# Performance work log

Measured on AMD Instinct MI355X. Metric: run time of the kernel, lower is better.

## Reference

```python
import jax, jax.numpy as jnp
import numpy as np

TOP_K = 8
ROUTED_SCALING = 2.5


def setup_inputs() -> dict:
    key = jax.random.key(0)
    ks = jax.random.split(key, 8)
    B, S, H, E, I = 2, 1024, 2048, 32, 1024
    IS = 2 * I  # shared expert intermediate (n_shared_experts * moe_intermediate_size)
    w = lambda k, shape: jax.random.normal(k, shape, dtype=jnp.float32) * 0.02
    return {
        "hidden_states": jax.random.normal(ks[0], (B, S, H), dtype=jnp.float32),
        "gate_weight": w(ks[1], (E, H)),
        "w_gate": w(ks[2], (E, H, I)),
        "w_up": w(ks[3], (E, H, I)),
        "w_down": w(ks[4], (E, I, H)),
        "ws_gate": w(ks[5], (H, IS)),
        "ws_up": w(ks[6], (H, IS)),
        "ws_down": w(ks[7], (IS, H)),
    }


def reference(hidden_states, gate_weight, w_gate, w_up, w_down, ws_gate, ws_up, ws_down):
    B, S, H = hidden_states.shape
    x = hidden_states.reshape(-1, H)  # [T, H]
    T = x.shape[0]
    E = gate_weight.shape[0]

    # --- gate (DeepseekV3 top-k router: sigmoid scores, top-k, renormalize, scale) ---
    scores = jax.nn.sigmoid(x @ gate_weight.T)              # [T, E]
    topk_w, topk_i = jax.lax.top_k(scores, TOP_K)           # [T, K]
    topk_w = topk_w / (jnp.sum(topk_w, axis=-1, keepdims=True) + 1e-20)
    topk_w = topk_w * ROUTED_SCALING

    # dense [T, E] combine weights (scatter of top-k weights; zeros elsewhere)
    dense_w = jnp.zeros((T, E), dtype=topk_w.dtype).at[
        jnp.arange(T)[:, None], topk_i
    ].add(topk_w)

    # --- all experts on all tokens (calibrate_all_experts semantics; non-selected get weight 0) ---
    g = jnp.einsum('th,ehi->eti', x, w_gate)                # [E, T, I]
    u = jnp.einsum('th,ehi->eti', x, w_up)                  # [E, T, I]
    eo = jnp.einsum('eti,eih->eth', jax.nn.silu(g) * u, w_down)  # [E, T, H]
    routed = jnp.einsum('eth,te->th', eo, dense_w)          # weighted scatter-combine

    # --- shared expert (gated SiLU MLP on residual) ---
    shared = (jax.nn.silu(x @ ws_gate) * (x @ ws_up)) @ ws_down

    return (routed + shared).reshape(B, S, H)
```

## Files before the change

### kernel.cpp

```cpp
#include <hip/hip_runtime.h>

#define T_TOK 2048
#define H_DIM 2048
#define E_NUM 32
#define I_DIM 1024
#define IS_DIM 2048
#define K_TOT (E_NUM * I_DIM + IS_DIM)
#define SLOT_CAP 2048
#define NE_ALL 34
#define GU_TILES 192
#define DN_TILES 176
#define ACT_SLOTS 24576

typedef __bf16 bf16x8 __attribute__((ext_vector_type(8)));
typedef float  f32x4  __attribute__((ext_vector_type(4)));
static_assert(sizeof(bf16x8) == 16, "bf16x8 must be 16B");

#define OFF_CNT   ((size_t)0)
#define OFF_NTGU  ((size_t)192)
#define OFF_NTDN  ((size_t)196)
#define OFF_BASE  ((size_t)256)
#define OFF_TGU   ((size_t)512)
#define OFF_TDN   ((size_t)1280)
#define OFF_PAIRS ((size_t)2048)
#define OFF_XB    ((size_t)280576)
#define OFF_WGT   ((size_t)8669184)
#define OFF_WUT   ((size_t)142886912)
#define OFF_WSGT  ((size_t)277104640)
#define OFF_WSUT  ((size_t)285493248)
#define OFF_WDT   ((size_t)293881856)
#define OFF_ACT   ((size_t)436488192)

__device__ __forceinline__ unsigned short f2bf(float f) {
  unsigned int u = __float_as_uint(f);
  u += 0x7fffu + ((u >> 16) & 1u);
  return (unsigned short)(u >> 16);
}

__device__ __forceinline__ void gld16(const void* g, void* l) {
  __builtin_amdgcn_global_load_lds(
      (const __attribute__((address_space(1))) unsigned int*)g,
      (__attribute__((address_space(3))) unsigned int*)l, 16, 0, 0);
}

__global__ __launch_bounds__(256) void router_kernel(
    const float* __restrict__ x, const float* __restrict__ gw,
    int* __restrict__ cnt, unsigned int* __restrict__ pairs,
    unsigned short* __restrict__ xb)
{
  const int t = blockIdx.x;
  __shared__ float xs[H_DIM];
  __shared__ float sc[E_NUM];
  const float4* xr = (const float4*)(x + (long)t * H_DIM);
  for (int i = threadIdx.x; i < H_DIM / 4; i += 256) ((float4*)xs)[i] = xr[i];
  __syncthreads();
  {
    const int i0 = threadIdx.x * 8;
    ushort4 o1, o2;
    o1.x = f2bf(xs[i0 + 0]); o1.y = f2bf(xs[i0 + 1]);
    o1.z = f2bf(xs[i0 + 2]); o1.w = f2bf(xs[i0 + 3]);
    o2.x = f2bf(xs[i0 + 4]); o2.y = f2bf(xs[i0 + 5]);
    o2.z = f2bf(xs[i0 + 6]); o2.w = f2bf(xs[i0 + 7]);
    *(ushort4*)(xb + (long)t * H_DIM + i0) = o1;
    *(ushort4*)(xb + (long)t * H_DIM + i0 + 4) = o2;
  }
  const int e = threadIdx.x >> 3, p = threadIdx.x & 7;
  const float4* ga = (const float4*)(gw + (long)e * H_DIM);
  const float4* xa = (const float4*)xs;
  float s = 0.f;
  #pragma unroll 4
  for (int i = p * 64; i < p * 64 + 64; ++i) {
    float4 a = ga[i], b = xa[i];
    s += a.x * b.x + a.y * b.y + a.z * b.z + a.w * b.w;
  }
  s += __shfl_down(s, 4, 8);
  s += __shfl_down(s, 2, 8);
  s += __shfl_down(s, 1, 8);
  if (p == 0) sc[e] = 1.f / (1.f + expf(-s));
  __syncthreads();
  if (threadIdx.x == 0) {
    float v[E_NUM];
    #pragma unroll
    for (int i = 0; i < E_NUM; ++i) v[i] = sc[i];
    unsigned mask = 0; float sum = 0.f;
    int sel[8]; float wv[8];
    for (int k = 0; k < 8; ++k) {
      float best = -1.f; int bi = 0;
      for (int i = 0; i < E_NUM; ++i)
        if (!((mask >> i) & 1u) && v[i] > best) { best = v[i]; bi = i; }
      mask |= 1u << bi; sel[k] = bi; wv[k] = best; sum += best;
    }
    const float scale = 2.5f / (sum + 1e-20f);
    for (int k = 0; k < 8; ++k) {
      const int slot = atomicAdd(&cnt[sel[k]], 1);
      if (slot < SLOT_CAP) {
        const unsigned int w16 = (unsigned int)f2bf(wv[k] * scale);
        pairs[sel[k] * SLOT_CAP + slot] = (w16 << 16) | (unsigned int)t;
      }
    }
  }
}

__global__ __launch_bounds__(256) void build_tiles_kernel(
    int* __restrict__ cnt, int* __restrict__ base,
    unsigned int* __restrict__ tgu, int* __restrict__ ntgu,
    unsigned int* __restrict__ tdn, int* __restrict__ ntdn,
    unsigned int* __restrict__ pairs)
{
  const int t = threadIdx.x;
  for (int s = t; s < T_TOK; s += 256) {
    const unsigned int pv = (0x3F80u << 16) | (unsigned int)s;
    pairs[32 * SLOT_CAP + s] = pv;
    pairs[33 * SLOT_CAP + s] = pv;
  }
  if (t == 0) {
    cnt[32] = T_TOK; cnt[33] = T_TOK;
    int b = 0, ngu = 0, ndn = 0;
    for (int e = 0; e < NE_ALL; ++e) {
      const int c = (e < 32) ? cnt[e] : T_TOK;
      base[e] = b;
      for (int m0 = 0; m0 < c; m0 += 128) {
        tgu[ngu++] = ((unsigned int)e << 16) | (unsigned int)m0;
        if (e < 33) tdn[ndn++] = ((unsigned int)e << 16) | (unsigned int)m0;
      }
      b += (c + 127) & ~127;
    }
    *ntgu = ngu; *ntdn = ndn;
  }
}

struct TDescTable {
  const float* in[6];
  unsigned short* out[6];
  int C[6];
  int ldout[6];
  long in_bs[6];
  long out_bs[6];
  int nbx[6];
  int nbxy[6];
  int start[7];
};

__global__ __launch_bounds__(256) void transpose_fused(TDescTable td)
{
  const int bid = blockIdx.x;
  int i = 0;
  while (i < 5 && bid >= td.start[i + 1]) ++i;
  const int local = bid - td.start[i];
  const int bz = local / td.nbxy[i];
  const int rem = local % td.nbxy[i];
  const int by = rem / td.nbx[i];
  const int bx = rem % td.nbx[i];
  const float* in = td.in[i] + (long)bz * td.in_bs[i];
  unsigned short* out = td.out[i] + (long)bz * td.out_bs[i];
  const int C = td.C[i], ldout = td.ldout[i];

  __shared__ unsigned short tile[64][258];
  const int c0 = bx * 64;
  const int r0 = by * 256;
  const int t = threadIdx.x;
  const int rl0 = t >> 4;
  const int cl0 = (t & 15) * 4;

  float4 v[16];
  #pragma unroll
  for (int p = 0; p < 16; ++p) {
    const int rl = p * 16 + rl0;
    v[p] = *(const float4*)(in + (long)(r0 + rl) * C + c0 + cl0);
  }
  __builtin_amdgcn_sched_barrier(0);
  #pragma unroll
  for (int p = 0; p < 16; ++p) {
    const int rl = p * 16 + rl0;
    tile[cl0 + 0][rl] = f2bf(v[p].x);
    tile[cl0 + 1][rl] = f2bf(v[p].y);
    tile[cl0 + 2][rl] = f2bf(v[p].z);
    tile[cl0 + 3][rl] = f2bf(v[p].w);
  }
  __syncthreads();
  const int cw = t >> 5;
  const int rw = (t & 31) * 8;
  #pragma unroll
  for (int q = 0; q < 8; ++q) {
    const int cl = q * 8 + cw;
    const char* src = (const char*)&tile[cl][rw];
    uint4 o;
    o.x = *(const unsigned int*)(src + 0);
    o.y = *(const unsigned int*)(src + 4);
    o.z = *(const unsigned int*)(src + 8);
    o.w = *(const unsigned int*)(src + 12);
    *(uint4*)(out + (long)(c0 + cl) * ldout + r0 + rw) = o;
  }
}

__global__ __launch_bounds__(256) void gate_up_moe_kernel(
    const unsigned short* __restrict__ xb,
    const unsigned short* __restrict__ bgT,
    const unsigned short* __restrict__ buT,
    const unsigned short* __restrict__ sgT,
    const unsigned short* __restrict__ suT,
    const int* __restrict__ cnt,
    const int* __restrict__ base,
    const unsigned int* __restrict__ pairs,
    const unsigned int* __restrict__ tiles,
    const int* __restrict__ ntp,
    unsigned short* __restrict__ act)
{
  const int ti = blockIdx.y;
  if (ti >= *ntp) return;
  const unsigned int tile = tiles[ti];
  const int e  = (int)(tile >> 16);
  const int m0 = (int)(tile & 0xFFFFu);
  const int cnte = cnt[e];
  const int be = base[e];
  const int n0 = blockIdx.x * 64;
  const long panel = (long)I_DIM * H_DIM;
  const unsigned short* Bg =
      ((e < 32) ? bgT + e * panel : sgT + (e - 32) * panel) + (long)n0 * H_DIM;
  const unsigned short* Bu =
      ((e < 32) ? buT + e * panel : suT + (e - 32) * panel) + (long)n0 * H_DIM;

  __shared__ unsigned short sA[128 * 64];
  __shared__ unsigned short sBg[64 * 64];
  __shared__ unsigned short sBu[64 * 64];

  const int tid = threadIdx.x;
  const int lane = tid & 63;
  const int wid = tid >> 6;
  const int wm = wid >> 1, wn = wid & 1;
  const int l15 = lane & 15;
  const int lk  = (lane >> 4) * 8;
  const int srow = tid >> 3;
  const int scol = (tid & 7) * 8;
  const int scolsw = (((tid & 7) ^ (srow & 7))) * 8;
  const int ksw = (l15 & 7) << 3;

  const unsigned short* asrc[4];
  #pragma unroll
  for (int r = 0; r < 4; ++r) {
    const int slot = m0 + r * 32 + srow;
    const unsigned int pr = (slot < cnte) ? pairs[e * SLOT_CAP + slot] : 0u;
    asrc[r] = xb + (long)(pr & 0xFFFFu) * H_DIM + scolsw;
  }

  const f32x4 fz = {0.f, 0.f, 0.f, 0.f};
  f32x4 accg[4][2], accu[4][2];
  #pragma unroll
  for (int i = 0; i < 4; ++i)
    #pragma unroll
    for (int j = 0; j < 2; ++j) { accg[i][j] = fz; accu[i][j] = fz; }

  for (int k0 = 0; k0 < H_DIM; k0 += 64) {
    #pragma unroll
    for (int r = 0; r < 4; ++r)
      gld16(asrc[r] + k0, sA + (r * 32 + srow) * 64 + scol);
    #pragma unroll
    for (int r = 0; r < 2; ++r) {
      gld16(Bg + (long)(r * 32 + srow) * H_DIM + k0 + scolsw,
            sBg + (r * 32 + srow) * 64 + scol);
      gld16(Bu + (long)(r * 32 + srow) * H_DIM + k0 + scolsw,
            sBu + (r * 32 + srow) * 64 + scol);
    }
    __syncthreads();
    __builtin_amdgcn_s_setprio(1);
    #pragma unroll
    for (int kk = 0; kk < 2; ++kk) {
      const int ko = kk * 32 + lk;
      bf16x8 a[4], g[2], u[2];
      #pragma unroll
      for (int mi = 0; mi < 4; ++mi)
        a[mi] = *(const bf16x8*)(sA + (wm * 64 + mi * 16 + l15) * 64 + (ko ^ ksw));
      #pragma unroll
      for (int ni = 0; ni < 2; ++ni) {
        g[ni] = *(const bf16x8*)(sBg + (wn * 32 + ni * 16 + l15) * 64 + (ko ^ ksw));
        u[ni] = *(const bf16x8*)(sBu + (wn * 32 + ni * 16 + l15) * 64 + (ko ^ ksw));
      }
      #pragma unroll
      for (int mi = 0; mi < 4; ++mi)
        #pragma unroll
        for (int ni = 0; ni < 2; ++ni) {
          accg[mi][ni] = __builtin_amdgcn_mfma_f32_16x16x32_bf16(a[mi], g[ni], accg[mi][ni], 0, 0, 0);
          accu[mi][ni] = __builtin_amdgcn_mfma_f32_16x16x32_bf16(a[mi], u[ni], accu[mi][ni], 0, 0, 0);
        }
    }
    __builtin_amdgcn_s_setprio(0);
    __syncthreads();
  }

  const int colb = n0 + wn * 32;
  #pragma unroll
  for (int mi = 0; mi < 4; ++mi) {
    #pragma unroll
    for (int r = 0; r < 4; ++r) {
      const int slot = m0 + wm * 64 + mi * 16 + (lane >> 4) * 4 + r;
      if (slot < cnte) {
        const unsigned int pr = pairs[e * SLOT_CAP + slot];
        const float w = __uint_as_float(pr & 0xFFFF0000u);
        #pragma unroll
        for (int ni = 0; ni < 2; ++ni) {
          const float gv = accg[mi][ni][r];
          const float uv = accu[mi][ni][r];
          const float sv = (gv / (1.f + expf(-gv))) * uv * w;
          act[((long)(be + slot)) * I_DIM + colb + ni * 16 + l15] = f2bf(sv);
        }
      }
    }
  }
}

__global__ __launch_bounds__(256) void down_moe_kernel(
    const unsigned short* __restrict__ act,
    const unsigned short* __restrict__ wdT,
    const int* __restrict__ cnt,
    const int* __restrict__ base,
    const unsigned int* __restrict__ pairs,
    const unsigned int* __restrict__ tiles,
    const int* __restrict__ ntp,
    float* __restrict__ out)
{
  const int ti = blockIdx.y;
  if (ti >= *ntp) return;
  const unsigned int tile = tiles[ti];
  const int e  = (int)(tile >> 16);
  const int m0 = (int)(tile & 0xFFFFu);
  const int cnte = cnt[e];
  const int n0 = blockIdx.x * 128;
  const unsigned short* A = act + ((long)base[e] + m0) * I_DIM;
  const unsigned short* B = wdT + (long)n0 * K_TOT + (long)e * I_DIM;
  const int nk = (e == 32) ? 32 : 16;

  __shared__ unsigned short sA[128 * 64];
  __shared__ unsigned short sB[128 * 64];

  const int tid = threadIdx.x;
  const int lane = tid & 63;
  const int wid = tid >> 6;
  const int wm = wid >> 1, wn = wid & 1;
  const int l15 = lane & 15;
  const int lk  = (lane >> 4) * 8;
  const int srow = tid >> 3;
  const int scol = (tid & 7) * 8;
  const int scolsw = (((tid & 7) ^ (srow & 7))) * 8;
  const int ksw = (l15 & 7) << 3;

  const f32x4 fz = {0.f, 0.f, 0.f, 0.f};
  f32x4 acc[4][4];
  #pragma unroll
  for (int i = 0; i < 4; ++i)
    #pragma unroll
    for (int j = 0; j < 4; ++j) acc[i][j] = fz;

  for (int t = 0; t < nk; ++t) {
    const int k0 = t * 64;
    const long koff = (long)(k0 & 1023) + (long)(k0 >> 10) * (2048L * 1024L);
    #pragma unroll
    for (int r = 0; r < 4; ++r)
      gld16(A + (long)(r * 32 + srow) * I_DIM + koff + scolsw,
            sA + (r * 32 + srow) * 64 + scol);
    #pragma unroll
    for (int r = 0; r < 4; ++r)
      gld16(B + (long)(r * 32 + srow) * K_TOT + k0 + scolsw,
            sB + (r * 32 + srow) * 64 + scol);
    __syncthreads();
    __builtin_amdgcn_s_setprio(1);
    #pragma unroll
    for (int kk = 0; kk < 2; ++kk) {
      const int ko = kk * 32 + lk;
      bf16x8 a[4], b[4];
      #pragma unroll
      for (int mi = 0; mi < 4; ++mi)
        a[mi] = *(const bf16x8*)(sA + (wm * 64 + mi * 16 + l15) * 64 + (ko ^ ksw));
      #pragma unroll
      for (int ni = 0; ni < 4; ++ni)
        b[ni] = *(const bf16x8*)(sB + (wn * 64 + ni * 16 + l15) * 64 + (ko ^ ksw));
      #pragma unroll
      for (int mi = 0; mi < 4; ++mi)
        #pragma unroll
        for (int ni = 0; ni < 4; ++ni)
          acc[mi][ni] = __builtin_amdgcn_mfma_f32_16x16x32_bf16(a[mi], b[ni], acc[mi][ni], 0, 0, 0);
    }
    __builtin_amdgcn_s_setprio(0);
    __syncthreads();
  }

  #pragma unroll
  for (int mi = 0; mi < 4; ++mi) {
    #pragma unroll
    for (int r = 0; r < 4; ++r) {
      const int slot = m0 + wm * 64 + mi * 16 + (lane >> 4) * 4 + r;
      if (slot < cnte) {
        const int tok = (int)(pairs[e * SLOT_CAP + slot] & 0xFFFFu);
        #pragma unroll
        for (int ni = 0; ni < 4; ++ni)
          atomicAdd(out + (long)tok * H_DIM + n0 + wn * 64 + ni * 16 + l15,
                    acc[mi][ni][r]);
      }
    }
  }
}

extern "C" void kernel_launch(void* const* d_in, const int* in_sizes, int n_in,
                              void* d_out, int out_size, void* d_ws, size_t ws_size,
                              hipStream_t stream) {
  (void)in_sizes; (void)n_in; (void)ws_size;
  const float* x   = (const float*)d_in[0];
  const float* gw  = (const float*)d_in[1];
  const float* wg  = (const float*)d_in[2];
  const float* wu  = (const float*)d_in[3];
  const float* wd  = (const float*)d_in[4];
  const float* wsg = (const float*)d_in[5];
  const float* wsu = (const float*)d_in[6];
  const float* wsd = (const float*)d_in[7];
  float* out = (float*)d_out;
  char* ws = (char*)d_ws;

  int*            cnt   = (int*)(ws + OFF_CNT);
  int*            ntgu  = (int*)(ws + OFF_NTGU);
  int*            ntdn  = (int*)(ws + OFF_NTDN);
  int*            basep = (int*)(ws + OFF_BASE);
  unsigned int*   tgu   = (unsigned int*)(ws + OFF_TGU);
  unsigned int*   tdn   = (unsigned int*)(ws + OFF_TDN);
  unsigned int*   pairs = (unsigned int*)(ws + OFF_PAIRS);
  unsigned short* xb    = (unsigned short*)(ws + OFF_XB);
  unsigned short* wgT   = (unsigned short*)(ws + OFF_WGT);
  unsigned short* wuT   = (unsigned short*)(ws + OFF_WUT);
  unsigned short* wsgT  = (unsigned short*)(ws + OFF_WSGT);
  unsigned short* wsuT  = (unsigned short*)(ws + OFF_WSUT);
  unsigned short* wdT   = (unsigned short*)(ws + OFF_WDT);
  unsigned short* actb  = (unsigned short*)(ws + OFF_ACT);

  hipMemsetAsync(ws + OFF_CNT, 0, 256, stream);
  hipMemsetAsync(out, 0, (size_t)out_size * sizeof(float), stream);

  router_kernel<<<T_TOK, 256, 0, stream>>>(x, gw, cnt, pairs, xb);
  build_tiles_kernel<<<1, 256, 0, stream>>>(cnt, basep, tgu, ntgu, tdn, ntdn,
                                            pairs);

  TDescTable ta;
  ta.in[0] = wg;  ta.out[0] = wgT;  ta.C[0] = I_DIM;  ta.ldout[0] = H_DIM;
  ta.in_bs[0] = (long)H_DIM * I_DIM; ta.out_bs[0] = (long)I_DIM * H_DIM;
  ta.nbx[0] = I_DIM / 64; ta.nbxy[0] = (I_DIM / 64) * (H_DIM / 256);
  ta.in[1] = wu;  ta.out[1] = wuT;  ta.C[1] = I_DIM;  ta.ldout[1] = H_DIM;
  ta.in_bs[1] = (long)H_DIM * I_DIM; ta.out_bs[1] = (long)I_DIM * H_DIM;
  ta.nbx[1] = I_DIM / 64; ta.nbxy[1] = (I_DIM / 64) * (H_DIM / 256);
  ta.in[2] = wsg; ta.out[2] = wsgT; ta.C[2] = IS_DIM; ta.ldout[2] = H_DIM;
  ta.in_bs[2] = 0; ta.out_bs[2] = 0;
  ta.nbx[2] = IS_DIM / 64; ta.nbxy[2] = (IS_DIM / 64) * (H_DIM / 256);
  ta.in[3] = wsu; ta.out[3] = wsuT; ta.C[3] = IS_DIM; ta.ldout[3] = H_DIM;
  ta.in_bs[3] = 0; ta.out_bs[3] = 0;
  ta.nbx[3] = IS_DIM / 64; ta.nbxy[3] = (IS_DIM / 64) * (H_DIM / 256);
  ta.in[4] = wsu; ta.out[4] = wsuT; ta.C[4] = IS_DIM; ta.ldout[4] = H_DIM;
  ta.in_bs[4] = 0; ta.out_bs[4] = 0; ta.nbx[4] = 1; ta.nbxy[4] = 1;
  ta.in[5] = ta.in[4]; ta.out[5] = ta.out[4]; ta.C[5] = ta.C[4];
  ta.ldout[5] = ta.ldout[4]; ta.in_bs[5] = 0; ta.out_bs[5] = 0;
  ta.nbx[5] = 1; ta.nbxy[5] = 1;
  ta.start[0] = 0;
  ta.start[1] = ta.start[0] + ta.nbxy[0] * E_NUM;
  ta.start[2] = ta.start[1] + ta.nbxy[1] * E_NUM;
  ta.start[3] = ta.start[2] + ta.nbxy[2];
  ta.start[4] = ta.start[3] + ta.nbxy[3];
  ta.start[5] = ta.start[4];
  ta.start[6] = ta.start[5];
  transpose_fused<<<ta.start[6] == ta.start[4] ? ta.start[4] : ta.start[6],
                    256, 0, stream>>>(ta);

  gate_up_moe_kernel<<<dim3(16, GU_TILES), 256, 0, stream>>>(
      xb, wgT, wuT, wsgT, wsuT, cnt, basep, pairs, tgu, ntgu, actb);

  TDescTable tb;
  tb.in[0] = wd;  tb.out[0] = wdT;  tb.C[0] = H_DIM;  tb.ldout[0] = K_TOT;
  tb.in_bs[0] = (long)I_DIM * H_DIM; tb.out_bs[0] = (long)I_DIM;
  tb.nbx[0] = H_DIM / 64; tb.nbxy[0] = (H_DIM / 64) * (I_DIM / 256);
  tb.in[1] = wsd; tb.out[1] = wdT + E_NUM * I_DIM; tb.C[1] = H_DIM;
  tb.ldout[1] = K_TOT; tb.in_bs[1] = 0; tb.out_bs[1] = 0;
  tb.nbx[1] = H_DIM / 64; tb.nbxy[1] = (H_DIM / 64) * (IS_DIM / 256);
  for (int i = 2; i < 6; ++i) {
    tb.in[i] = tb.in[1]; tb.out[i] = tb.out[1]; tb.C[i] = tb.C[1];
    tb.ldout[i] = tb.ldout[1]; tb.in_bs[i] = 0; tb.out_bs[i] = 0;
    tb.nbx[i] = 1; tb.nbxy[i] = 1;
  }
  tb.start[0] = 0;
  tb.start[1] = tb.start[0] + tb.nbxy[0] * E_NUM;
  tb.start[2] = tb.start[1] + tb.nbxy[1];
  tb.start[3] = tb.start[2];
  tb.start[4] = tb.start[2];
  tb.start[5] = tb.start[2];
  tb.start[6] = tb.start[2];
  transpose_fused<<<tb.start[6], 256, 0, stream>>>(tb);

  down_moe_kernel<<<dim3(16, DN_TILES), 256, 0, stream>>>(
      actb, wdT, cnt, basep, pairs, tdn, ntdn, out);
}
```

Baseline: 833.1 us.

## Replace atomic scatter-add in down projection with bf16 partials and combine kernel

After: 753.4 us. 9.6% less time.

```diff
diff --git a/kernel.cpp b/kernel.cpp
--- a/kernel.cpp
+++ b/kernel.cpp
@@ -25,11 +25,13 @@
 #define OFF_PAIRS ((size_t)2048)
 #define OFF_XB    ((size_t)280576)
 #define OFF_WGT   ((size_t)8669184)
+#define OFF_PO    OFF_WGT
 #define OFF_WUT   ((size_t)142886912)
 #define OFF_WSGT  ((size_t)277104640)
 #define OFF_WSUT  ((size_t)285493248)
 #define OFF_WDT   ((size_t)293881856)
 #define OFF_ACT   ((size_t)436488192)
+#define OFF_TSLOT ((size_t)486819840)
 
 __device__ __forceinline__ unsigned short f2bf(float f) {
   unsigned int u = __float_as_uint(f);
@@ -46,7 +48,7 @@
 __global__ __launch_bounds__(256) void router_kernel(
     const float* __restrict__ x, const float* __restrict__ gw,
     int* __restrict__ cnt, unsigned int* __restrict__ pairs,
-    unsigned short* __restrict__ xb)
+    unsigned int* __restrict__ tslot, unsigned short* __restrict__ xb)
 {
   const int t = blockIdx.x;
   __shared__ float xs[H_DIM];
@@ -96,6 +98,7 @@
       if (slot < SLOT_CAP) {
         const unsigned int w16 = (unsigned int)f2bf(wv[k] * scale);
         pairs[sel[k] * SLOT_CAP + slot] = (w16 << 16) | (unsigned int)t;
+        tslot[t * 8 + k] = ((unsigned int)sel[k] << 16) | (unsigned int)slot;
       }
     }
   }
@@ -313,10 +316,9 @@
     const unsigned short* __restrict__ wdT,
     const int* __restrict__ cnt,
     const int* __restrict__ base,
-    const unsigned int* __restrict__ pairs,
     const unsigned int* __restrict__ tiles,
     const int* __restrict__ ntp,
-    float* __restrict__ out)
+    unsigned short* __restrict__ po)
 {
   const int ti = blockIdx.y;
   if (ti >= *ntp) return;
@@ -324,8 +326,9 @@
   const int e  = (int)(tile >> 16);
   const int m0 = (int)(tile & 0xFFFFu);
   const int cnte = cnt[e];
+  const int be = base[e];
   const int n0 = blockIdx.x * 128;
-  const unsigned short* A = act + ((long)base[e] + m0) * I_DIM;
+  const unsigned short* A = act + ((long)be + m0) * I_DIM;
   const unsigned short* B = wdT + (long)n0 * K_TOT + (long)e * I_DIM;
   const int nk = (e == 32) ? 32 : 16;
 
@@ -389,20 +392,56 @@
     for (int r = 0; r < 4; ++r) {
       const int slot = m0 + wm * 64 + mi * 16 + (lane >> 4) * 4 + r;
       if (slot < cnte) {
-        const int tok = (int)(pairs[e * SLOT_CAP + slot] & 0xFFFFu);
+        unsigned short* pr = po + (long)(be + slot) * H_DIM + n0 + wn * 64;
         #pragma unroll
         for (int ni = 0; ni < 4; ++ni)
-          atomicAdd(out + (long)tok * H_DIM + n0 + wn * 64 + ni * 16 + l15,
-                    acc[mi][ni][r]);
+          pr[ni * 16 + l15] = f2bf(acc[mi][ni][r]);
       }
     }
   }
+}
+
+__global__ __launch_bounds__(256) void combine_kernel(
+    const unsigned short* __restrict__ po,
+    const int* __restrict__ base,
+    const unsigned int* __restrict__ tslot,
+    float* __restrict__ out)
+{
+  const int t = blockIdx.x;
+  __shared__ int rows[9];
+  if (threadIdx.x < 8) {
+    const unsigned int pr = tslot[t * 8 + threadIdx.x];
+    rows[threadIdx.x] = base[pr >> 16] + (int)(pr & 0xFFFFu);
+  }
+  if (threadIdx.x == 8) rows[8] = base[32] + t;
+  __syncthreads();
+  const int col = threadIdx.x * 8;
+  float s[8];
+  #pragma unroll
+  for (int j = 0; j < 8; ++j) s[j] = 0.f;
+  #pragma unroll
+  for (int k = 0; k < 9; ++k) {
+    const ushort4* p = (const ushort4*)(po + (long)rows[k] * H_DIM + col);
+    const ushort4 v0 = p[0], v1 = p[1];
+    s[0] += __uint_as_float((unsigned int)v0.x << 16);
+    s[1] += __uint_as_float((unsigned int)v0.y << 16);
+    s[2] += __uint_as_float((unsigned int)v0.z << 16);
+    s[3] += __uint_as_float((unsigned int)v0.w << 16);
+    s[4] += __uint_as_float((unsigned int)v1.x << 16);
+    s[5] += __uint_as_float((unsigned int)v1.y << 16);
+    s[6] += __uint_as_float((unsigned int)v1.z << 16);
+    s[7] += __uint_as_float((unsigned int)v1.w << 16);
+  }
+  float4 o0 = {s[0], s[1], s[2], s[3]};
+  float4 o1 = {s[4], s[5], s[6], s[7]};
+  *(float4*)(out + (long)t * H_DIM + col) = o0;
+  *(float4*)(out + (long)t * H_DIM + col + 4) = o1;
 }
 
 extern "C" void kernel_launch(void* const* d_in, const int* in_sizes, int n_in,
                               void* d_out, int out_size, void* d_ws, size_t ws_size,
                               hipStream_t stream) {
-  (void)in_sizes; (void)n_in; (void)ws_size;
+  (void)in_sizes; (void)n_in; (void)out_size; (void)ws_size;
   const float* x   = (const float*)d_in[0];
   const float* gw  = (const float*)d_in[1];
   const float* wg  = (const float*)d_in[2];
@@ -421,6 +460,7 @@
   unsigned int*   tgu   = (unsigned int*)(ws + OFF_TGU);
   unsigned int*   tdn   = (unsigned int*)(ws + OFF_TDN);
   unsigned int*   pairs = (unsigned int*)(ws + OFF_PAIRS);
+  unsigned int*   tslot = (unsigned int*)(ws + OFF_TSLOT);
   unsigned short* xb    = (unsigned short*)(ws + OFF_XB);
   unsigned short* wgT   = (unsigned short*)(ws + OFF_WGT);
   unsigned short* wuT   = (unsigned short*)(ws + OFF_WUT);
@@ -428,11 +468,11 @@
   unsigned short* wsuT  = (unsigned short*)(ws + OFF_WSUT);
   unsigned short* wdT   = (unsigned short*)(ws + OFF_WDT);
   unsigned short* actb  = (unsigned short*)(ws + OFF_ACT);
+  unsigned short* pob   = (unsigned short*)(ws + OFF_PO);
 
   hipMemsetAsync(ws + OFF_CNT, 0, 256, stream);
-  hipMemsetAsync(out, 0, (size_t)out_size * sizeof(float), stream);
-
-  router_kernel<<<T_TOK, 256, 0, stream>>>(x, gw, cnt, pairs, xb);
+
+  router_kernel<<<T_TOK, 256, 0, stream>>>(x, gw, cnt, pairs, tslot, xb);
   build_tiles_kernel<<<1, 256, 0, stream>>>(cnt, basep, tgu, ntgu, tdn, ntdn,
                                             pairs);
 
@@ -449,20 +489,19 @@
   ta.in[3] = wsu; ta.out[3] = wsuT; ta.C[3] = IS_DIM; ta.ldout[3] = H_DIM;
   ta.in_bs[3] = 0; ta.out_bs[3] = 0;
   ta.nbx[3] = IS_DIM / 64; ta.nbxy[3] = (IS_DIM / 64) * (H_DIM / 256);
-  ta.in[4] = wsu; ta.out[4] = wsuT; ta.C[4] = IS_DIM; ta.ldout[4] = H_DIM;
-  ta.in_bs[4] = 0; ta.out_bs[4] = 0; ta.nbx[4] = 1; ta.nbxy[4] = 1;
-  ta.in[5] = ta.in[4]; ta.out[5] = ta.out[4]; ta.C[5] = ta.C[4];
-  ta.ldout[5] = ta.ldout[4]; ta.in_bs[5] = 0; ta.out_bs[5] = 0;
-  ta.nbx[5] = 1; ta.nbxy[5] = 1;
+  for (int i = 4; i < 6; ++i) {
+    ta.in[i] = ta.in[3]; ta.out[i] = ta.out[3]; ta.C[i] = ta.C[3];
+    ta.ldout[i] = ta.ldout[3]; ta.in_bs[i] = 0; ta.out_bs[i] = 0;
+    ta.nbx[i] = 1; ta.nbxy[i] = 1;
+  }
   ta.start[0] = 0;
   ta.start[1] = ta.start[0] + ta.nbxy[0] * E_NUM;
   ta.start[2] = ta.start[1] + ta.nbxy[1] * E_NUM;
   ta.start[3] = ta.start[2] + ta.nbxy[2];
   ta.start[4] = ta.start[3] + ta.nbxy[3];
   ta.start[5] = ta.start[4];
-  ta.start[6] = ta.start[5];
-  transpose_fused<<<ta.start[6] == ta.start[4] ? ta.start[4] : ta.start[6],
-                    256, 0, stream>>>(ta);
+  ta.start[6] = ta.start[4];
+  transpose_fused<<<ta.start[4], 256, 0, stream>>>(ta);
 
   gate_up_moe_kernel<<<dim3(16, GU_TILES), 256, 0, stream>>>(
       xb, wgT, wuT, wsgT, wsuT, cnt, basep, pairs, tgu, ntgu, actb);
@@ -486,8 +525,10 @@
   tb.start[4] = tb.start[2];
   tb.start[5] = tb.start[2];
   tb.start[6] = tb.start[2];
-  transpose_fused<<<tb.start[6], 256, 0, stream>>>(tb);
+  transpose_fused<<<tb.start[2], 256, 0, stream>>>(tb);
 
   down_moe_kernel<<<dim3(16, DN_TILES), 256, 0, stream>>>(
-      actb, wdT, cnt, basep, pairs, tdn, ntdn, out);
-}
+      actb, wdT, cnt, basep, tdn, ntdn, pob);
+
+  combine_kernel<<<T_TOK, 256, 0, stream>>>(pob, basep, tslot, out);
+}
```
